# Kernel optimization log

Hardware: AMD Instinct MI355X
Metric: run time of the kernel (lower is better)

Reference implementation:

```python
import math
import jax, jax.numpy as jnp
import numpy as np

B, S, D, H, F = 2, 2048, 1024, 16, 4096
HD = D // H
EPS = 1e-6
ALPHA, BETA = 0.5, 1.0  # SpectralActivation defaults


def setup_inputs() -> dict:
    key = jax.random.key(0)
    ks = jax.random.split(key, 24)
    init = lambda k, shape: (jax.random.normal(k, shape, jnp.float32) * 0.02)
    return {
        "x": jax.random.normal(ks[0], (B, S, D), jnp.float32),
        # attention params (W stored as [in, out], i.e. y = x @ W + b)
        "Wq": init(ks[1], (D, D)), "bq": jnp.zeros((D,), jnp.float32),
        "Wk": init(ks[2], (D, D)), "bk": jnp.zeros((D,), jnp.float32),
        "Wv": init(ks[3], (D, D)), "bv": jnp.zeros((D,), jnp.float32),
        "Wo": init(ks[4], (D, D)), "bo": jnp.zeros((D,), jnp.float32),
        "resonance": jnp.ones((H, 1, 1), jnp.float32),
        "phase": jnp.zeros((H, 1, 1), jnp.float32),
        # norm1
        "g1": jnp.ones((D,), jnp.float32), "b1": jnp.zeros((D,), jnp.float32),
        "s1": jnp.full((1,), 0.1, jnp.float32),
        # FFN
        "W1": init(ks[5], (D, F)), "bf1": jnp.zeros((F,), jnp.float32),
        "W2": init(ks[6], (F, D)), "bf2": jnp.zeros((D,), jnp.float32),
        # norm2
        "g2": jnp.ones((D,), jnp.float32), "b2": jnp.zeros((D,), jnp.float32),
        "s2": jnp.full((1,), 0.1, jnp.float32),
    }


def _harmonic_ln(x, gamma, beta, stab):
    mean = jnp.mean(x, axis=-1, keepdims=True)
    std = jnp.std(x, axis=-1, keepdims=True, ddof=1)  # torch std is unbiased
    std = std + stab * jnp.sin(std * math.pi)
    return gamma * ((x - mean) / (std + EPS)) + beta


def _spectral_act(x):
    c = math.sqrt(2.0 / math.pi)
    gelu_like = 0.5 * x * (1.0 + jnp.tanh(c * (x + 0.044715 * x ** 3)))
    return gelu_like + ALPHA * jnp.sin(BETA * x)


def _forward(x, Wq, bq, Wk, bk, Wv, bv, Wo, bo, resonance, phase,
             g1, b1, s1, W1, bf1, W2, bf2, g2, b2, s2):
    Bq, Sq, _ = x.shape
    q = (x @ Wq + bq).reshape(Bq, Sq, H, HD).transpose(0, 2, 1, 3)  # [B,H,S,hd]
    k = (x @ Wk + bk).reshape(Bq, Sq, H, HD).transpose(0, 2, 1, 3)
    v = (x @ Wv + bv).reshape(Bq, Sq, H, HD).transpose(0, 2, 1, 3)

    scores = jnp.einsum('bhqd,bhkd->bhqk', q, k) / math.sqrt(HD)  # [B,H,S,S]
    scores = scores + resonance[None] * jnp.sin(scores + phase[None])
    attn = jax.nn.softmax(scores, axis=-1)
    out = jnp.einsum('bhqk,bhkd->bhqd', attn, v)
    out = out.transpose(0, 2, 1, 3).reshape(Bq, Sq, D)
    attn_out = out @ Wo + bo

    x = _harmonic_ln(x + attn_out, g1, b1, s1)
    ff = _spectral_act(x @ W1 + bf1) @ W2 + bf2
    x = _harmonic_ln(x + ff, g2, b2, s2)
    return x


def reference(x, Wq, bq, Wk, bk, Wv, bv, Wo, bo, resonance, phase,
              g1, b1, s1, W1, bf1, W2, bf2, g2, b2, s2):
    return _forward(x, Wq, bq, Wk, bk, Wv, bv, Wo, bo, resonance, phase,
                    g1, b1, s1, W1, bf1, W2, bf2, g2, b2, s2)
```

## Files before the change

kernel.cpp:

```cpp
#include <hip/hip_runtime.h>
#include <cstdint>
#include <cstddef>


typedef float  f32x4  __attribute__((ext_vector_type(4)));
typedef __bf16 bf16x8 __attribute__((ext_vector_type(8)));
typedef unsigned short u16x8 __attribute__((ext_vector_type(8)));
typedef unsigned short u16x4 __attribute__((ext_vector_type(4)));
typedef unsigned int   u32x2 __attribute__((ext_vector_type(2)));
typedef unsigned int   u32x4 __attribute__((ext_vector_type(4)));

#define MFMA_BF16(a, b, c) __builtin_amdgcn_mfma_f32_16x16x32_bf16((a), (b), (c), 0, 0, 0)

static __device__ __forceinline__ unsigned short f32_to_bf16(float f) {
  return __builtin_bit_cast(unsigned short, (__bf16)f);
}
static __device__ __forceinline__ bf16x8 lds_frag(const unsigned short* base, int byte) {
  return __builtin_bit_cast(bf16x8, *(const u16x8*)((const char*)base + byte));
}
static __device__ __forceinline__ float spectral_act(float x) {
  const float c = 0.7978845608028654f;
  float g = 0.5f * x * (1.0f + tanhf(c * (x + 0.044715f * x * x * x)));
  return g + 0.5f * __sinf(x);
}
static __device__ __forceinline__ void gload_lds16(const void* g, void* lds) {
  __builtin_amdgcn_global_load_lds((const __attribute__((address_space(1))) unsigned int*)g,
                                   (__attribute__((address_space(3))) unsigned int*)lds,
                                   16, 0, 0);
}
static __device__ __forceinline__ u32x2 tr_read(unsigned addr) {
  u32x2 r;
  asm volatile("ds_read_b64_tr_b16 %0, %1" : "=v"(r) : "v"(addr));
  return r;
}

__global__ __launch_bounds__(256) void cvt_f32_bf16(const float* __restrict__ in,
                                                    unsigned short* __restrict__ out, int n) {
  int i = (blockIdx.x * 256 + threadIdx.x) * 4;
  if (i < n) {
    float4 v = *(const float4*)(in + i);
    u16x4 o;
    o[0] = f32_to_bf16(v.x); o[1] = f32_to_bf16(v.y);
    o[2] = f32_to_bf16(v.z); o[3] = f32_to_bf16(v.w);
    *(u16x4*)(out + i) = o;
  }
}

__global__ __launch_bounds__(256) void transpose_f32_bf16(const float* __restrict__ W,
                                                          unsigned short* __restrict__ Wt,
                                                          int K, int N) {
  __shared__ float tile[32][33];
  int tx = threadIdx.x & 31, ty = threadIdx.x >> 5;
  int k0 = blockIdx.y * 32, n0 = blockIdx.x * 32;
#pragma unroll
  for (int i = 0; i < 4; i++)
    tile[ty + i * 8][tx] = W[(size_t)(k0 + ty + i * 8) * N + n0 + tx];
  __syncthreads();
#pragma unroll
  for (int i = 0; i < 4; i++)
    Wt[(size_t)(n0 + ty + i * 8) * K + k0 + tx] = f32_to_bf16(tile[tx][ty + i * 8]);
}

template <int EPI>
__global__ __launch_bounds__(512, 2) void gemm_bt8(const unsigned short* __restrict__ Ag,
                                                   const unsigned short* __restrict__ Bt,
                                                   const float* __restrict__ bias,
                                                   unsigned short* __restrict__ Cb,
                                                   float* __restrict__ Cf,
                                                   int M, int N, int K) {
  __shared__ unsigned short As[2][256 * 64];
  __shared__ unsigned short Bs[2][256 * 64];
  const int t = threadIdx.x;
  const int lane = t & 63, w = t >> 6;
  const int wr = w >> 2, wc = w & 3;
  const int g = lane >> 4, cc = lane & 15;
  const int row0 = blockIdx.y * 256, col0 = blockIdx.x * 256;

  f32x4 acc[8][4];
#pragma unroll
  for (int mi = 0; mi < 8; mi++)
#pragma unroll
    for (int ni = 0; ni < 4; ni++) acc[mi][ni] = (f32x4){0.f, 0.f, 0.f, 0.f};

  const int nk = K >> 6;
  const int sro8 = w * 8 + (lane >> 3);
  const int sc8 = ((lane & 7) ^ ((lane >> 3) & 7)) * 8;

  auto stageA = [&](int buf, int kt, int h) {
#pragma unroll
    for (int i = 0; i < 2; ++i) {
      int rr = h * 128 + i * 64 + sro8;
      gload_lds16(Ag + (size_t)(row0 + rr) * K + (kt << 6) + sc8,
                  &As[buf][(h * 128 + i * 64 + w * 8) * 64]);
    }
  };
  auto stageB = [&](int buf, int kt, int h) {
#pragma unroll
    for (int i = 0; i < 2; ++i) {
      int rr = h * 128 + i * 64 + sro8;
      gload_lds16(Bt + (size_t)(col0 + rr) * K + (kt << 6) + sc8,
                  &Bs[buf][(h * 128 + i * 64 + w * 8) * 64]);
    }
  };
  auto rdA = [&](int buf, int qm, bf16x8 a[2][4]) {
#pragma unroll
    for (int ks = 0; ks < 2; ++ks)
#pragma unroll
      for (int i = 0; i < 4; ++i) {
        int r = wr * 128 + (qm * 4 + i) * 16 + cc;
        a[ks][i] = lds_frag(&As[buf][0], r * 128 + (((ks * 4 + g) ^ (cc & 7)) << 4));
      }
  };
  auto rdB = [&](int buf, int qn, bf16x8 bb[2][2]) {
#pragma unroll
    for (int ks = 0; ks < 2; ++ks)
#pragma unroll
      for (int j = 0; j < 2; ++j) {
        int r = wc * 64 + (qn * 2 + j) * 16 + cc;
        bb[ks][j] = lds_frag(&Bs[buf][0], r * 128 + (((ks * 4 + g) ^ (cc & 7)) << 4));
      }
  };
  auto mma = [&](int qm, int qn, bf16x8 a[2][4], bf16x8 bb[2][2]) {
    __builtin_amdgcn_s_setprio(1);
#pragma unroll
    for (int ks = 0; ks < 2; ++ks)
#pragma unroll
      for (int i = 0; i < 4; ++i)
#pragma unroll
        for (int j = 0; j < 2; ++j)
          acc[qm * 4 + i][qn * 2 + j] =
              MFMA_BF16(a[ks][i], bb[ks][j], acc[qm * 4 + i][qn * 2 + j]);
    __builtin_amdgcn_s_setprio(0);
  };

#define SYNC_IN()  do { asm volatile("s_barrier" ::: "memory");               \
                        asm volatile("s_waitcnt lgkmcnt(0)" ::: "memory");    \
                        __builtin_amdgcn_sched_barrier(0); } while (0)
#define SYNC_OUT() asm volatile("s_barrier" ::: "memory")

  stageA(0, 0, 0); stageA(0, 0, 1); stageB(0, 0, 0); stageB(0, 0, 1);
  if (nk > 1) {
    stageA(1, 1, 0);
    asm volatile("s_waitcnt vmcnt(2)" ::: "memory");
  } else {
    asm volatile("s_waitcnt vmcnt(0)" ::: "memory");
  }
  asm volatile("s_barrier" ::: "memory");

  const int niter = nk >> 1;
  for (int j = 0; j < niter; ++j) {
    const int t0 = 2 * j, t1 = 2 * j + 1;
    const bool s0 = (t0 + 2 < nk), s1 = (t1 + 2 < nk);
    bf16x8 a[2][4], bb0[2][2], bb1[2][2];

    rdA(0, 0, a); rdB(0, 0, bb0);
    stageA(1, t1, 1);
    SYNC_IN(); mma(0, 0, a, bb0); SYNC_OUT();
    rdB(0, 1, bb1);
    stageB(1, t1, 0);
    SYNC_IN(); mma(0, 1, a, bb1); SYNC_OUT();
    rdA(0, 1, a);
    stageB(1, t1, 1);
    SYNC_IN(); mma(1, 1, a, bb1); SYNC_OUT();
    rdB(0, 0, bb0);
    if (s0) { stageA(0, t0 + 2, 0); asm volatile("s_waitcnt vmcnt(2)" ::: "memory"); }
    else    {                       asm volatile("s_waitcnt vmcnt(0)" ::: "memory"); }
    SYNC_IN(); mma(1, 0, a, bb0); SYNC_OUT();

    rdA(1, 0, a); rdB(1, 0, bb0);
    if (s0) stageA(0, t0 + 2, 1);
    SYNC_IN(); mma(0, 0, a, bb0); SYNC_OUT();
    rdB(1, 1, bb1);
    if (s0) stageB(0, t0 + 2, 0);
    SYNC_IN(); mma(0, 1, a, bb1); SYNC_OUT();
    rdA(1, 1, a);
    if (s0) stageB(0, t0 + 2, 1);
    SYNC_IN(); mma(1, 1, a, bb1); SYNC_OUT();
    rdB(1, 0, bb0);
    if (s1) { stageA(1, t1 + 2, 0); asm volatile("s_waitcnt vmcnt(2)" ::: "memory"); }
    SYNC_IN(); mma(1, 0, a, bb0); SYNC_OUT();
  }
#undef SYNC_IN
#undef SYNC_OUT

#pragma unroll
  for (int mi = 0; mi < 8; ++mi) {
#pragma unroll
    for (int ni = 0; ni < 4; ++ni) {
      int col = col0 + wc * 64 + ni * 16 + cc;
      float bv = bias[col];
#pragma unroll
      for (int r4 = 0; r4 < 4; r4++) {
        int row = row0 + wr * 128 + mi * 16 + g * 4 + r4;
        float val = acc[mi][ni][r4] + bv;
        if (EPI == 2) val = spectral_act(val);
        if (EPI == 0 || EPI == 2) Cb[(size_t)row * N + col] = f32_to_bf16(val);
        else                      Cf[(size_t)row * N + col] = val;
      }
    }
  }
}

template <int BM, int BN, int EPI>
__global__ __launch_bounds__(256) void gemm_bt(const unsigned short* __restrict__ A,
                                               const unsigned short* __restrict__ Bt,
                                               const float* __restrict__ bias,
                                               unsigned short* __restrict__ Cb,
                                               float* __restrict__ Cf,
                                               int M, int N, int K) {
  constexpr int MI = BM / 32;
  constexpr int NI = BN / 32;
  __shared__ unsigned short As[2][BM * 32];
  __shared__ unsigned short Bs[2][BN * 32];
  const int t = threadIdx.x;
  const int lane = t & 63, w = t >> 6;
  const int wr = w >> 1, wc = w & 1;
  const int g = lane >> 4, cc = lane & 15;
  const int row0 = blockIdx.y * BM, col0 = blockIdx.x * BN;

  f32x4 acc[MI][NI];
#pragma unroll
  for (int mi = 0; mi < MI; mi++)
#pragma unroll
    for (int ni = 0; ni < NI; ni++) acc[mi][ni] = (f32x4){0.f, 0.f, 0.f, 0.f};

  const int nk = K >> 5;
  const int srow = lane >> 2;
  const int schunk = (lane & 3) ^ (srow & 3);

  auto stage = [&](int buf, int kt) {
#pragma unroll
    for (int i = 0; i < BM / 64; ++i) {
      int r = i * 64 + w * 16;
      gload_lds16(A + (size_t)(row0 + r + srow) * K + (kt << 5) + schunk * 8,
                  &As[buf][r * 32]);
    }
#pragma unroll
    for (int i = 0; i < BN / 64; ++i) {
      int r = i * 64 + w * 16;
      gload_lds16(Bt + (size_t)(col0 + r + srow) * K + (kt << 5) + schunk * 8,
                  &Bs[buf][r * 32]);
    }
  };

  stage(0, 0);
  __syncthreads();
  int cur = 0;
  for (int kt = 0; kt < nk; ++kt) {
    if (kt + 1 < nk) stage(cur ^ 1, kt + 1);

    bf16x8 af[MI], bg[NI];
#pragma unroll
    for (int mi = 0; mi < MI; mi++) {
      int r = wr * (BM / 2) + mi * 16 + cc;
      af[mi] = lds_frag(&As[cur][0], r * 64 + ((g ^ (cc & 3)) << 4));
    }
#pragma unroll
    for (int ni = 0; ni < NI; ni++) {
      int r = wc * (BN / 2) + ni * 16 + cc;
      bg[ni] = lds_frag(&Bs[cur][0], r * 64 + ((g ^ (cc & 3)) << 4));
    }
#pragma unroll
    for (int mi = 0; mi < MI; mi++)
#pragma unroll
      for (int ni = 0; ni < NI; ni++)
        acc[mi][ni] = MFMA_BF16(af[mi], bg[ni], acc[mi][ni]);

    __syncthreads();
    cur ^= 1;
  }

#pragma unroll
  for (int mi = 0; mi < MI; mi++) {
#pragma unroll
    for (int ni = 0; ni < NI; ni++) {
      int col = col0 + wc * (BN / 2) + ni * 16 + cc;
      float bv = bias[col];
#pragma unroll
      for (int r4 = 0; r4 < 4; r4++) {
        int row = row0 + wr * (BM / 2) + mi * 16 + g * 4 + r4;
        float val = acc[mi][ni][r4] + bv;
        if (EPI == 2) val = spectral_act(val);
        if (EPI == 0 || EPI == 2) Cb[(size_t)row * N + col] = f32_to_bf16(val);
        else                      Cf[(size_t)row * N + col] = val;
      }
    }
  }
}

__global__ __launch_bounds__(256) void attn_fused(const unsigned short* __restrict__ Qb,
                                                  const unsigned short* __restrict__ Kb,
                                                  const unsigned short* __restrict__ Vb,
                                                  int ld,
                                                  const float* __restrict__ resonance,
                                                  const float* __restrict__ phase,
                                                  unsigned short* __restrict__ O, int ldo) {
  constexpr int S = 2048;
  __shared__ unsigned short Ks[64 * 64];
  __shared__ unsigned short Vs[4][64 * 16];
  __shared__ unsigned short Ps[4][16 * 64];

  const int t = threadIdx.x, lane = t & 63, w = t >> 6;
  const int g = lane >> 4, cc = lane & 15;
  const int bh = blockIdx.y, b = bh >> 4, h = bh & 15;
  const int q0 = blockIdx.x * 64 + w * 16;
  const float res = resonance[h], ph = phase[h];

  const unsigned short* Qh = Qb + (size_t)b * S * ld + h * 64;
  const unsigned short* Kh = Kb + (size_t)b * S * ld + h * 64;
  const unsigned short* Vh = Vb + (size_t)b * S * ld + h * 64;

  bf16x8 qa0, qa1;
  {
    const unsigned short* qp = Qh + (size_t)(q0 + cc) * ld + g * 8;
    qa0 = __builtin_bit_cast(bf16x8, *(const u16x8*)qp);
    qa1 = __builtin_bit_cast(bf16x8, *(const u16x8*)(qp + 32));
  }

  bf16x8 ones8;
#pragma unroll
  for (int j = 0; j < 8; j++) ones8[j] = (__bf16)1.0f;

  const int krow = t >> 3, kc8 = (t & 7) * 8;
  const int vkey = t & 63, vb0 = (t >> 6) * 16;
  u16x8 kr0, kr1, vr0, vr1;

  auto issue_loads = [&](int kt) {
    const unsigned short* kp = Kh + (size_t)(kt * 64) * ld;
    kr0 = *(const u16x8*)(kp + (size_t)krow * ld + kc8);
    kr1 = *(const u16x8*)(kp + (size_t)(krow + 32) * ld + kc8);
    const unsigned short* vp = Vh + (size_t)(kt * 64 + vkey) * ld + vb0;
    vr0 = *(const u16x8*)vp;
    vr1 = *(const u16x8*)(vp + 8);
  };
  auto stage_lds = [&]() {
    *(u16x8*)((char*)Ks + ((krow * 128 + kc8 * 2) ^ ((krow & 7) << 4))) = kr0;
    int row2 = krow + 32;
    *(u16x8*)((char*)Ks + ((row2 * 128 + kc8 * 2) ^ ((row2 & 7) << 4))) = kr1;
    int sw = (vkey >> 3) & 1;
    char* vb = (char*)&Vs[t >> 6][0] + vkey * 32;
    *(u16x8*)(vb + sw * 16) = vr0;
    *(u16x8*)(vb + (1 - sw) * 16) = vr1;
  };

  const unsigned vs_base = (unsigned)(uintptr_t)(void*)&Vs[0][0];
  const unsigned tr_a = vs_base + (unsigned)((8 * g + (cc >> 2)) * 32 +
                                             (((cc & 2) >> 1) ^ (g & 1)) * 16 +
                                             (cc & 1) * 8);

  f32x4 oacc[4];
#pragma unroll
  for (int i = 0; i < 4; i++) oacc[i] = (f32x4){0.f, 0.f, 0.f, 0.f};
  float Mx[4] = {-1e30f, -1e30f, -1e30f, -1e30f};
  float Lx[4] = {0.f, 0.f, 0.f, 0.f};
  char* PsW = (char*)&Ps[w][0];

  issue_loads(0);
  for (int kt = 0; kt < S / 64; ++kt) {
    stage_lds();
    __syncthreads();
    if (kt + 1 < S / 64) issue_loads(kt + 1);

    f32x4 sacc[4];
#pragma unroll
    for (int nb = 0; nb < 4; nb++) sacc[nb] = (f32x4){0.f, 0.f, 0.f, 0.f};
#pragma unroll
    for (int nb = 0; nb < 4; nb++) {
      int key = nb * 16 + cc;
      int rb = key * 128, xr = (key & 7) << 4;
      bf16x8 k0 = lds_frag(Ks, (rb + g * 16) ^ xr);
      bf16x8 k1 = lds_frag(Ks, (rb + 64 + g * 16) ^ xr);
      sacc[nb] = MFMA_BF16(qa0, k0, sacc[nb]);
      sacc[nb] = MFMA_BF16(qa1, k1, sacc[nb]);
    }

    float sm[4] = {-1e30f, -1e30f, -1e30f, -1e30f};
#pragma unroll
    for (int nb = 0; nb < 4; nb++)
#pragma unroll
      for (int r4 = 0; r4 < 4; r4++) {
        float sv = sacc[nb][r4] * 0.125f;
        sv += res * __sinf(sv + ph);
        sacc[nb][r4] = sv;
        sm[r4] = fmaxf(sm[r4], sv);
      }
#pragma unroll
    for (int d = 1; d < 16; d <<= 1)
#pragma unroll
      for (int r4 = 0; r4 < 4; r4++) sm[r4] = fmaxf(sm[r4], __shfl_xor(sm[r4], d, 16));

    float alpha[4];
#pragma unroll
    for (int r4 = 0; r4 < 4; r4++) {
      float nm = fmaxf(Mx[r4], sm[r4]);
      alpha[r4] = __expf(Mx[r4] - nm);
      Mx[r4] = nm;
    }
#pragma unroll
    for (int nb = 0; nb < 4; nb++)
#pragma unroll
      for (int r4 = 0; r4 < 4; r4++) {
        float p = __expf(sacc[nb][r4] - Mx[r4]);
        int prow = g * 4 + r4, pcol = nb * 16 + cc;
        *(unsigned short*)(PsW + ((prow * 128 + pcol * 2) ^ ((prow & 7) << 4))) =
            f32_to_bf16(p);
      }

    bf16x8 pa0, pa1;
    {
      int xr = (cc & 7) << 4;
      pa0 = lds_frag((const unsigned short*)PsW, (cc * 128 + g * 16) ^ xr);
      pa1 = lds_frag((const unsigned short*)PsW, (cc * 128 + 64 + g * 16) ^ xr);
    }
    f32x4 pacc = (f32x4){0.f, 0.f, 0.f, 0.f};
    pacc = MFMA_BF16(pa0, ones8, pacc);
    pacc = MFMA_BF16(pa1, ones8, pacc);
#pragma unroll
    for (int r4 = 0; r4 < 4; r4++) Lx[r4] = Lx[r4] * alpha[r4] + pacc[r4];
#pragma unroll
    for (int nb2 = 0; nb2 < 4; nb2++)
#pragma unroll
      for (int r4 = 0; r4 < 4; r4++) oacc[nb2][r4] *= alpha[r4];

    u32x2 trv[4][4];
#pragma unroll
    for (int b2 = 0; b2 < 4; b2++) {
      unsigned a = tr_a + b2 * 2048;
      trv[b2][0] = tr_read(a);
      trv[b2][1] = tr_read(a + 128);
      trv[b2][2] = tr_read(a + 1024);
      trv[b2][3] = tr_read(a + 1152);
    }
    asm volatile("s_waitcnt lgkmcnt(0)" ::: "memory");
    __builtin_amdgcn_sched_barrier(0);
#pragma unroll
    for (int b2 = 0; b2 < 4; b2++) {
      bf16x8 v0 = __builtin_bit_cast(bf16x8,
          (u32x4){trv[b2][0][0], trv[b2][0][1], trv[b2][1][0], trv[b2][1][1]});
      bf16x8 v1 = __builtin_bit_cast(bf16x8,
          (u32x4){trv[b2][2][0], trv[b2][2][1], trv[b2][3][0], trv[b2][3][1]});
      oacc[b2] = MFMA_BF16(pa0, v0, oacc[b2]);
      oacc[b2] = MFMA_BF16(pa1, v1, oacc[b2]);
    }
    __syncthreads();
  }

#pragma unroll
  for (int nb2 = 0; nb2 < 4; nb2++)
#pragma unroll
    for (int r4 = 0; r4 < 4; r4++) {
      float ov = oacc[nb2][r4] / Lx[r4];
      O[(size_t)(b * S + q0 + g * 4 + r4) * ldo + h * 64 + nb2 * 16 + cc] = f32_to_bf16(ov);
    }
}

__global__ __launch_bounds__(256) void resid_harmonic_ln(const float* __restrict__ xin,
                                                         const float* __restrict__ radd,
                                                         const float* __restrict__ gamma,
                                                         const float* __restrict__ beta,
                                                         const float* __restrict__ stab,
                                                         float* __restrict__ yf,
                                                         unsigned short* __restrict__ yb) {
  const int row = blockIdx.x, t = threadIdx.x;
  const float* xr = xin + (size_t)row * 1024;
  const float* rr = radd + (size_t)row * 1024;
  float v[4], s = 0.f, ss = 0.f;
#pragma unroll
  for (int j = 0; j < 4; j++) {
    int idx = t + j * 256;
    v[j] = xr[idx] + rr[idx];
    s += v[j]; ss += v[j] * v[j];
  }
#pragma unroll
  for (int d = 1; d < 64; d <<= 1) { s += __shfl_xor(s, d); ss += __shfl_xor(ss, d); }
  __shared__ float sb[8];
  int lane = t & 63, wid = t >> 6;
  if (lane == 0) { sb[wid] = s; sb[4 + wid] = ss; }
  __syncthreads();
  s = sb[0] + sb[1] + sb[2] + sb[3];
  ss = sb[4] + sb[5] + sb[6] + sb[7];
  float mean = s * (1.f / 1024.f);
  float var = fmaxf((ss - 1024.f * mean * mean) * (1.f / 1023.f), 0.f);
  float sd = sqrtf(var);
  sd += stab[0] * sinf(sd * 3.14159265358979323846f);
  float inv = 1.f / (sd + 1e-6f);
#pragma unroll
  for (int j = 0; j < 4; j++) {
    int idx = t + j * 256;
    float y = gamma[idx] * ((v[j] - mean) * inv) + beta[idx];
    yf[(size_t)row * 1024 + idx] = y;
    if (yb) yb[(size_t)row * 1024 + idx] = f32_to_bf16(y);
  }
}

extern "C" void kernel_launch(void* const* d_in, const int* in_sizes, int n_in,
                              void* d_out, int out_size, void* d_ws, size_t ws_size,
                              hipStream_t stream) {
  const float* x    = (const float*)d_in[0];
  const float* Wq   = (const float*)d_in[1];
  const float* bq   = (const float*)d_in[2];
  const float* Wk   = (const float*)d_in[3];
  const float* bk   = (const float*)d_in[4];
  const float* Wv   = (const float*)d_in[5];
  const float* bv   = (const float*)d_in[6];
  const float* Wo   = (const float*)d_in[7];
  const float* bo   = (const float*)d_in[8];
  const float* reso = (const float*)d_in[9];
  const float* phas = (const float*)d_in[10];
  const float* g1   = (const float*)d_in[11];
  const float* b1   = (const float*)d_in[12];
  const float* s1   = (const float*)d_in[13];
  const float* W1   = (const float*)d_in[14];
  const float* bf1  = (const float*)d_in[15];
  const float* W2   = (const float*)d_in[16];
  const float* bf2  = (const float*)d_in[17];
  const float* g2   = (const float*)d_in[18];
  const float* b2   = (const float*)d_in[19];
  const float* s2   = (const float*)d_in[20];

  const int BS = 4096;

  char* ws = (char*)d_ws;
  const size_t OFF_QKV  = 0;
  const size_t OFF_XB   = 25165824;
  const size_t OFF_WQKV = 33554432;
  const size_t OFF_WOT  = 39845888;
  const size_t OFF_W1T  = 41943040;
  const size_t OFF_W2T  = 50331648;
  const size_t OFF_BQKV = 58720256;
  const size_t OFF_T0   = 58736640;
  const size_t OFF_X1   = 75513856;
  const size_t OFF_X1B  = 92291072;

  unsigned short* qkv   = (unsigned short*)(ws + OFF_QKV);
  unsigned short* xb    = (unsigned short*)(ws + OFF_XB);
  unsigned short* ao    = (unsigned short*)(ws + OFF_XB);
  unsigned short* Wqkvt = (unsigned short*)(ws + OFF_WQKV);
  unsigned short* Wot   = (unsigned short*)(ws + OFF_WOT);
  unsigned short* W1t   = (unsigned short*)(ws + OFF_W1T);
  unsigned short* W2t   = (unsigned short*)(ws + OFF_W2T);
  float*          bqkv  = (float*)(ws + OFF_BQKV);
  float*          t0    = (float*)(ws + OFF_T0);
  float*          x1    = (float*)(ws + OFF_X1);
  unsigned short* x1b   = (unsigned short*)(ws + OFF_X1B);
  unsigned short* hb    = (unsigned short*)(ws + OFF_QKV);
  float*          out   = (float*)d_out;

  cvt_f32_bf16<<<4096, 256, 0, stream>>>(x, xb, BS * 1024);

  transpose_f32_bf16<<<dim3(32, 32), 256, 0, stream>>>(Wq, Wqkvt, 1024, 1024);
  transpose_f32_bf16<<<dim3(32, 32), 256, 0, stream>>>(Wk, Wqkvt + (size_t)1024 * 1024, 1024, 1024);
  transpose_f32_bf16<<<dim3(32, 32), 256, 0, stream>>>(Wv, Wqkvt + (size_t)2048 * 1024, 1024, 1024);
  transpose_f32_bf16<<<dim3(32, 32), 256, 0, stream>>>(Wo, Wot, 1024, 1024);
  transpose_f32_bf16<<<dim3(128, 32), 256, 0, stream>>>(W1, W1t, 1024, 4096);
  transpose_f32_bf16<<<dim3(32, 128), 256, 0, stream>>>(W2, W2t, 4096, 1024);

  hipMemcpyAsync((void*)bqkv,          (const void*)bq, 1024 * 4, hipMemcpyDeviceToDevice, stream);
  hipMemcpyAsync((void*)(bqkv + 1024), (const void*)bk, 1024 * 4, hipMemcpyDeviceToDevice, stream);
  hipMemcpyAsync((void*)(bqkv + 2048), (const void*)bv, 1024 * 4, hipMemcpyDeviceToDevice, stream);

  gemm_bt8<0><<<dim3(12, 16), 512, 0, stream>>>(xb, Wqkvt, bqkv, qkv, nullptr,
                                                4096, 3072, 1024);

  attn_fused<<<dim3(32, 32), 256, 0, stream>>>(qkv, qkv + 1024, qkv + 2048, 3072,
                                               reso, phas, ao, 1024);

  gemm_bt<128, 64, 1><<<dim3(16, 32), 256, 0, stream>>>(ao, Wot, bo, nullptr, t0,
                                                        4096, 1024, 1024);

  resid_harmonic_ln<<<4096, 256, 0, stream>>>(x, t0, g1, b1, s1, x1, x1b);

  gemm_bt8<2><<<dim3(16, 16), 512, 0, stream>>>(x1b, W1t, bf1, hb, nullptr,
                                                4096, 4096, 1024);

  gemm_bt<128, 64, 1><<<dim3(16, 32), 256, 0, stream>>>(hb, W2t, bf2, nullptr, t0,
                                                        4096, 1024, 4096);

  resid_harmonic_ln<<<4096, 256, 0, stream>>>(x1, t0, g2, b2, s2, out, nullptr);
}
```

Before: 486.2 us.

## Split W2 GEMM over K into bf16 partials, vectorize LN, add setprio and fast sin

The K=4096 down-projection GEMM is split into four K=1024 launches that each write bf16 partial sums. The final layer norm then reduces the four partials together with the residual and bias. The layer-norm kernels are vectorized with float4 loads and stores. In attention, MFMA sections are wrapped in s_setprio and the sin uses a raw v_sin_f32. Storing partials in bf16 adds rounding error and more memory traffic, and the four launches still run serially on one stream.

```diff
diff --git a/kernel.cpp b/kernel.cpp
--- a/kernel.cpp
+++ b/kernel.cpp
@@ -15,6 +15,9 @@
 static __device__ __forceinline__ unsigned short f32_to_bf16(float f) {
   return __builtin_bit_cast(unsigned short, (__bf16)f);
 }
+static __device__ __forceinline__ float bf16_to_f32(unsigned short h) {
+  return __uint_as_float(((unsigned int)h) << 16);
+}
 static __device__ __forceinline__ bf16x8 lds_frag(const unsigned short* base, int byte) {
   return __builtin_bit_cast(bf16x8, *(const u16x8*)((const char*)base + byte));
 }
@@ -31,6 +34,11 @@
 static __device__ __forceinline__ u32x2 tr_read(unsigned addr) {
   u32x2 r;
   asm volatile("ds_read_b64_tr_b16 %0, %1" : "=v"(r) : "v"(addr));
+  return r;
+}
+static __device__ __forceinline__ float fast_sin(float x) {
+  float r;
+  asm("v_sin_f32 %0, %1" : "=v"(r) : "v"(x * 0.15915494309189535f));
   return r;
 }
 
@@ -203,7 +211,9 @@
 
 template <int BM, int BN, int EPI>
 __global__ __launch_bounds__(256) void gemm_bt(const unsigned short* __restrict__ A,
+                                               int lda,
                                                const unsigned short* __restrict__ Bt,
+                                               int ldb,
                                                const float* __restrict__ bias,
                                                unsigned short* __restrict__ Cb,
                                                float* __restrict__ Cf,
@@ -232,13 +242,13 @@
 #pragma unroll
     for (int i = 0; i < BM / 64; ++i) {
       int r = i * 64 + w * 16;
-      gload_lds16(A + (size_t)(row0 + r + srow) * K + (kt << 5) + schunk * 8,
+      gload_lds16(A + (size_t)(row0 + r + srow) * lda + (kt << 5) + schunk * 8,
                   &As[buf][r * 32]);
     }
 #pragma unroll
     for (int i = 0; i < BN / 64; ++i) {
       int r = i * 64 + w * 16;
-      gload_lds16(Bt + (size_t)(col0 + r + srow) * K + (kt << 5) + schunk * 8,
+      gload_lds16(Bt + (size_t)(col0 + r + srow) * ldb + (kt << 5) + schunk * 8,
                   &Bs[buf][r * 32]);
     }
   };
@@ -275,14 +285,14 @@
 #pragma unroll
     for (int ni = 0; ni < NI; ni++) {
       int col = col0 + wc * (BN / 2) + ni * 16 + cc;
-      float bv = bias[col];
+      float bv = (EPI == 3) ? 0.f : bias[col];
 #pragma unroll
       for (int r4 = 0; r4 < 4; r4++) {
         int row = row0 + wr * (BM / 2) + mi * 16 + g * 4 + r4;
         float val = acc[mi][ni][r4] + bv;
         if (EPI == 2) val = spectral_act(val);
-        if (EPI == 0 || EPI == 2) Cb[(size_t)row * N + col] = f32_to_bf16(val);
-        else                      Cf[(size_t)row * N + col] = val;
+        if (EPI == 0 || EPI == 2 || EPI == 3) Cb[(size_t)row * N + col] = f32_to_bf16(val);
+        else                                  Cf[(size_t)row * N + col] = val;
       }
     }
   }
@@ -364,6 +374,7 @@
     f32x4 sacc[4];
 #pragma unroll
     for (int nb = 0; nb < 4; nb++) sacc[nb] = (f32x4){0.f, 0.f, 0.f, 0.f};
+    __builtin_amdgcn_s_setprio(1);
 #pragma unroll
     for (int nb = 0; nb < 4; nb++) {
       int key = nb * 16 + cc;
@@ -373,6 +384,7 @@
       sacc[nb] = MFMA_BF16(qa0, k0, sacc[nb]);
       sacc[nb] = MFMA_BF16(qa1, k1, sacc[nb]);
     }
+    __builtin_amdgcn_s_setprio(0);
 
     float sm[4] = {-1e30f, -1e30f, -1e30f, -1e30f};
 #pragma unroll
@@ -380,7 +392,7 @@
 #pragma unroll
       for (int r4 = 0; r4 < 4; r4++) {
         float sv = sacc[nb][r4] * 0.125f;
-        sv += res * __sinf(sv + ph);
+        sv += res * fast_sin(sv + ph);
         sacc[nb][r4] = sv;
         sm[r4] = fmaxf(sm[r4], sv);
       }
@@ -433,6 +445,7 @@
     }
     asm volatile("s_waitcnt lgkmcnt(0)" ::: "memory");
     __builtin_amdgcn_sched_barrier(0);
+    __builtin_amdgcn_s_setprio(1);
 #pragma unroll
     for (int b2 = 0; b2 < 4; b2++) {
       bf16x8 v0 = __builtin_bit_cast(bf16x8,
@@ -442,6 +455,7 @@
       oacc[b2] = MFMA_BF16(pa0, v0, oacc[b2]);
       oacc[b2] = MFMA_BF16(pa1, v1, oacc[b2]);
     }
+    __builtin_amdgcn_s_setprio(0);
     __syncthreads();
   }
 
@@ -454,23 +468,11 @@
     }
 }
 
-__global__ __launch_bounds__(256) void resid_harmonic_ln(const float* __restrict__ xin,
-                                                         const float* __restrict__ radd,
-                                                         const float* __restrict__ gamma,
-                                                         const float* __restrict__ beta,
-                                                         const float* __restrict__ stab,
-                                                         float* __restrict__ yf,
-                                                         unsigned short* __restrict__ yb) {
-  const int row = blockIdx.x, t = threadIdx.x;
-  const float* xr = xin + (size_t)row * 1024;
-  const float* rr = radd + (size_t)row * 1024;
-  float v[4], s = 0.f, ss = 0.f;
-#pragma unroll
-  for (int j = 0; j < 4; j++) {
-    int idx = t + j * 256;
-    v[j] = xr[idx] + rr[idx];
-    s += v[j]; ss += v[j] * v[j];
-  }
+static __device__ __forceinline__ void harmonic_ln_tail(
+    float v[4], int row, int t, const float* gamma, const float* beta,
+    const float* stab, float* yf, unsigned short* yb) {
+  float s = v[0] + v[1] + v[2] + v[3];
+  float ss = v[0] * v[0] + v[1] * v[1] + v[2] * v[2] + v[3] * v[3];
 #pragma unroll
   for (int d = 1; d < 64; d <<= 1) { s += __shfl_xor(s, d); ss += __shfl_xor(ss, d); }
   __shared__ float sb[8];
@@ -484,13 +486,63 @@
   float sd = sqrtf(var);
   sd += stab[0] * sinf(sd * 3.14159265358979323846f);
   float inv = 1.f / (sd + 1e-6f);
+  float4 gv = ((const float4*)gamma)[t];
+  float4 bv = ((const float4*)beta)[t];
+  float4 y;
+  y.x = gv.x * ((v[0] - mean) * inv) + bv.x;
+  y.y = gv.y * ((v[1] - mean) * inv) + bv.y;
+  y.z = gv.z * ((v[2] - mean) * inv) + bv.z;
+  y.w = gv.w * ((v[3] - mean) * inv) + bv.w;
+  ((float4*)(yf + (size_t)row * 1024))[t] = y;
+  if (yb) {
+    u16x4 o;
+    o[0] = f32_to_bf16(y.x); o[1] = f32_to_bf16(y.y);
+    o[2] = f32_to_bf16(y.z); o[3] = f32_to_bf16(y.w);
+    ((u16x4*)(yb + (size_t)row * 1024))[t] = o;
+  }
+}
+
+__global__ __launch_bounds__(256) void resid_harmonic_ln(const float* __restrict__ xin,
+                                                         const float* __restrict__ radd,
+                                                         const float* __restrict__ gamma,
+                                                         const float* __restrict__ beta,
+                                                         const float* __restrict__ stab,
+                                                         float* __restrict__ yf,
+                                                         unsigned short* __restrict__ yb) {
+  const int row = blockIdx.x, t = threadIdx.x;
+  float4 xv = ((const float4*)(xin + (size_t)row * 1024))[t];
+  float4 rv = ((const float4*)(radd + (size_t)row * 1024))[t];
+  float v[4] = {xv.x + rv.x, xv.y + rv.y, xv.z + rv.z, xv.w + rv.w};
+  harmonic_ln_tail(v, row, t, gamma, beta, stab, yf, yb);
+}
+
+__global__ __launch_bounds__(256) void resid_harmonic_ln4(const float* __restrict__ xin,
+                                                          const unsigned short* __restrict__ p0,
+                                                          const unsigned short* __restrict__ p1,
+                                                          const unsigned short* __restrict__ p2,
+                                                          const unsigned short* __restrict__ p3,
+                                                          const float* __restrict__ rbias,
+                                                          const float* __restrict__ gamma,
+                                                          const float* __restrict__ beta,
+                                                          const float* __restrict__ stab,
+                                                          float* __restrict__ yf) {
+  const int row = blockIdx.x, t = threadIdx.x;
+  float4 xv = ((const float4*)(xin + (size_t)row * 1024))[t];
+  float4 bv = ((const float4*)rbias)[t];
+  u16x4 a0 = ((const u16x4*)(p0 + (size_t)row * 1024))[t];
+  u16x4 a1 = ((const u16x4*)(p1 + (size_t)row * 1024))[t];
+  u16x4 a2 = ((const u16x4*)(p2 + (size_t)row * 1024))[t];
+  u16x4 a3 = ((const u16x4*)(p3 + (size_t)row * 1024))[t];
+  float v[4];
 #pragma unroll
   for (int j = 0; j < 4; j++) {
-    int idx = t + j * 256;
-    float y = gamma[idx] * ((v[j] - mean) * inv) + beta[idx];
-    yf[(size_t)row * 1024 + idx] = y;
-    if (yb) yb[(size_t)row * 1024 + idx] = f32_to_bf16(y);
-  }
+    float r = bf16_to_f32(a0[j]) + bf16_to_f32(a1[j]) +
+              bf16_to_f32(a2[j]) + bf16_to_f32(a3[j]);
+    float xb = (j == 0) ? xv.x : (j == 1) ? xv.y : (j == 2) ? xv.z : xv.w;
+    float bb = (j == 0) ? bv.x : (j == 1) ? bv.y : (j == 2) ? bv.z : bv.w;
+    v[j] = xb + r + bb;
+  }
+  harmonic_ln_tail(v, row, t, gamma, beta, stab, yf, nullptr);
 }
 
 extern "C" void kernel_launch(void* const* d_in, const int* in_sizes, int n_in,
@@ -544,6 +596,10 @@
   float*          x1    = (float*)(ws + OFF_X1);
   unsigned short* x1b   = (unsigned short*)(ws + OFF_X1B);
   unsigned short* hb    = (unsigned short*)(ws + OFF_QKV);
+  unsigned short* p0    = (unsigned short*)(ws + OFF_T0);
+  unsigned short* p1    = (unsigned short*)(ws + OFF_T0 + 8388608);
+  unsigned short* p2    = (unsigned short*)(ws + OFF_X1B);
+  unsigned short* p3    = (unsigned short*)(ws + OFF_WQKV);
   float*          out   = (float*)d_out;
 
   cvt_f32_bf16<<<4096, 256, 0, stream>>>(x, xb, BS * 1024);
@@ -565,16 +621,21 @@
   attn_fused<<<dim3(32, 32), 256, 0, stream>>>(qkv, qkv + 1024, qkv + 2048, 3072,
                                                reso, phas, ao, 1024);
 
-  gemm_bt<128, 64, 1><<<dim3(16, 32), 256, 0, stream>>>(ao, Wot, bo, nullptr, t0,
-                                                        4096, 1024, 1024);
+  gemm_bt<128, 64, 1><<<dim3(16, 32), 256, 0, stream>>>(ao, 1024, Wot, 1024, bo,
+                                                        nullptr, t0, 4096, 1024, 1024);
 
   resid_harmonic_ln<<<4096, 256, 0, stream>>>(x, t0, g1, b1, s1, x1, x1b);
 
   gemm_bt8<2><<<dim3(16, 16), 512, 0, stream>>>(x1b, W1t, bf1, hb, nullptr,
                                                 4096, 4096, 1024);
 
-  gemm_bt<128, 64, 1><<<dim3(16, 32), 256, 0, stream>>>(hb, W2t, bf2, nullptr, t0,
-                                                        4096, 1024, 4096);
-
-  resid_harmonic_ln<<<4096, 256, 0, stream>>>(x1, t0, g2, b2, s2, out, nullptr);
-}
+  unsigned short* parts[4] = {p0, p1, p2, p3};
+  for (int z = 0; z < 4; ++z) {
+    gemm_bt<128, 64, 3><<<dim3(16, 32), 256, 0, stream>>>(
+        hb + (size_t)z * 1024, 4096, W2t + (size_t)z * 1024, 4096, nullptr,
+        parts[z], nullptr, 4096, 1024, 1024);
+  }
+
+  resid_harmonic_ln4<<<4096, 256, 0, stream>>>(x1, p0, p1, p2, p3, bf2,
+                                               g2, b2, s2, out);
+}
```

New measurement: 491.0 us. Within noise of the previous version (+1.0%).
